# Optimization experiments

Measured on AMD Instinct MI355X. Metric: run time of the kernel, lower is better.

The kernel has to match this reference:

```python
import jax, jax.numpy as jnp
import numpy as np

EPSILON = 1e-8
MAX_WEIGHT = 0.15
N_ITER = 20
STEP_SIZE = 0.05
B, P = 32768, 45


def _simplex_projection(w):
    # clamp + renormalize, done twice (differentiable approximation)
    w = jnp.clip(w, 0.0, MAX_WEIGHT)
    w = w / (jnp.sum(w, axis=-1, keepdims=True) + EPSILON)
    w = jnp.clip(w, 0.0, MAX_WEIGHT)
    w = w / (jnp.sum(w, axis=-1, keepdims=True) + EPSILON)
    return w


def setup_inputs() -> dict:
    key = jax.random.key(0)
    k1, k2 = jax.random.split(key, 2)
    # SPD-ish covariance for a well-behaved iterative solve
    A = jax.random.normal(k1, (B, P, P), dtype=jnp.float32) * 0.1
    sigma = jnp.einsum('bij,bkj->bik', A, A) + 0.1 * jnp.eye(P, dtype=jnp.float32)
    beta = jax.nn.softmax(jax.random.normal(k2, (B, P), dtype=jnp.float32), axis=-1)
    w_prev = jnp.full((B, P), 1.0 / P, dtype=jnp.float32)
    return {
        'sigma': sigma,
        'beta': beta,
        'w_prev': w_prev,
        'log_lambda_sparse': jnp.asarray(-3.0, dtype=jnp.float32),
        'log_lambda_turnover': jnp.asarray(-2.0, dtype=jnp.float32),
    }


def reference(sigma, beta, w_prev, log_lambda_sparse, log_lambda_turnover):
    Bb, Pp = beta.shape
    lam_s = jnp.exp(log_lambda_sparse)
    lam_t = jnp.exp(log_lambda_turnover)
    w0 = jnp.full((Bb, Pp), 1.0 / Pp, dtype=sigma.dtype)

    def step(w, _):
        Sw = jnp.einsum('bij,bj->bi', sigma, w)  # [B,P]
        grad = 2.0 * Sw - beta + lam_s * jnp.sign(w) + 2.0 * lam_t * (w - w_prev)
        w = _simplex_projection(w - STEP_SIZE * grad)
        return w, None

    w, _ = jax.lax.scan(step, w0, None, length=N_ITER)
    return w
```

## Files before the change

kernel.cpp:

```cpp
#include <hip/hip_runtime.h>
#include <math.h>

#define P 45
#define N_ITER 20

typedef float v2f __attribute__((ext_vector_type(2)));
typedef float v4f __attribute__((ext_vector_type(4)));

template<int CTRL>
__device__ __forceinline__ float dpp_add(float x) {
    int xi = __builtin_bit_cast(int, x);
    int yi = __builtin_amdgcn_update_dpp(0, xi, CTRL, 0xF, 0xF, true);
    return x + __builtin_bit_cast(float, yi);
}

__device__ __forceinline__ float wave_sum_bcast(float x) {
    x = dpp_add<0x111>(x);
    x = dpp_add<0x112>(x);
    x = dpp_add<0x114>(x);
    x = dpp_add<0x118>(x);
    x = dpp_add<0x142>(x);
    x = dpp_add<0x143>(x);
    int si = __builtin_amdgcn_readlane(__builtin_bit_cast(int, x), 63);
    return __builtin_bit_cast(float, si);
}

__device__ __forceinline__ float clamp015(float x) {
    return __builtin_amdgcn_fmed3f(x, 0.0f, 0.15f);
}

__global__ __launch_bounds__(64) void drb_kernel(
    const float* __restrict__ sigma,
    const float* __restrict__ beta,
    const float* __restrict__ w_prev,
    const float* __restrict__ lls,
    const float* __restrict__ llt,
    float* __restrict__ out)
{
    const int b    = blockIdx.x;
    const int lane = threadIdx.x;
    const bool active = lane < P;

    const float lam_s  = expf(lls[0]);
    const float lam_t2 = 2.0f * expf(llt[0]);

    float base = 0.0f;
    if (active) {
        base = -beta[(size_t)b * P + lane]
               - lam_t2 * w_prev[(size_t)b * P + lane];
    }

    const int cidx = active ? lane : 0;
    const float* sp = sigma + (size_t)b * (P * P) + cidx;
    float rv[P + 1];
    #pragma unroll
    for (int j = 0; j < P; ++j) {
        float v = sp[(size_t)j * P];
        rv[j] = active ? v : 0.0f;
    }
    rv[P] = 0.0f;
    const bool ones = (lane == P);
    v2f row2[23];
    #pragma unroll
    for (int k = 0; k < 23; ++k) {
        float lo = ones ? 1.0f : rv[2 * k];
        float hi = (2 * k + 1 < P) ? (ones ? 1.0f : rv[2 * k + 1]) : 0.0f;
        v2f t; t.x = lo; t.y = hi;
        row2[k] = t;
    }
    #pragma unroll
    for (int k = 0; k < 23; ++k) asm volatile("" : "+v"(row2[k]));

    __shared__ __align__(16) float sh[128];

    float c = active ? (float)(1.0 / 45.0) : 0.0f;

    for (int it = 0; it < N_ITER; ++it) {
        float* shb = sh + ((it & 1) << 6);
        shb[lane] = c;
        __syncthreads();
        const v4f* shv = (const v4f*)shb;

        v2f acc0; acc0.x = 0.0f; acc0.y = 0.0f;
        v2f acc1 = acc0, acc2 = acc0;
        #pragma unroll
        for (int k = 0; k < 11; ++k) {
            v4f q = shv[k];
            v2f lo; lo.x = q.x; lo.y = q.y;
            v2f hi; hi.x = q.z; hi.y = q.w;
            acc0 = __builtin_elementwise_fma(row2[2 * k],     lo, acc0);
            acc1 = __builtin_elementwise_fma(row2[2 * k + 1], hi, acc1);
        }
        {
            v4f q = shv[11];
            v2f lo; lo.x = q.x; lo.y = q.y;
            acc2 = __builtin_elementwise_fma(row2[22], lo, acc2);
        }
        v2f am = acc0 + acc1;
        am = am + acc2;
        const float acc = am.x + am.y;

        const float s2 = __builtin_bit_cast(float,
            __builtin_amdgcn_readlane(__builtin_bit_cast(int, acc), P));
        const float r = __builtin_amdgcn_rcpf(s2 + 1e-8f);

        const float t = c * r;
        float g = fmaf(lam_t2, t, base);
        g += (c > 0.0f) ? lam_s : 0.0f;
        g = fmaf(r + r, acc, g);
        const float x = fmaf(-0.05f, g, t);

        const float a  = clamp015(x);
        const float s1 = wave_sum_bcast(a);
        const float r1 = __builtin_amdgcn_rcpf(s1 + 1e-8f);
        c = clamp015(a * r1);
    }

    const float sf = wave_sum_bcast(c);
    const float rf = __builtin_amdgcn_rcpf(sf + 1e-8f);
    if (active) out[(size_t)b * P + lane] = c * rf;
}

extern "C" void kernel_launch(void* const* d_in, const int* in_sizes, int n_in,
                              void* d_out, int out_size, void* d_ws, size_t ws_size,
                              hipStream_t stream) {
    const float* sigma  = (const float*)d_in[0];
    const float* beta   = (const float*)d_in[1];
    const float* w_prev = (const float*)d_in[2];
    const float* lls    = (const float*)d_in[3];
    const float* llt    = (const float*)d_in[4];
    float* out = (float*)d_out;

    const int B = in_sizes[1] / P;
    drb_kernel<<<B, 64, 0, stream>>>(sigma, beta, w_prev, lls, llt, out);
}
```

Baseline: 376.1 us.

## Process eight batch elements per workgroup in a persistent loop

Each 64-thread workgroup now handles eight batch elements in sequence instead of one, so the grid shrinks eightfold. This is meant to amortise workgroup launch and setup costs such as the lambda exps. The dot product is also split over four accumulators instead of three to shorten FMA dependency chains. The risk is that the sigma loads for each element are no longer overlapped by other resident workgroups unless occupancy is high, so memory latency may be exposed serially.

```diff
diff --git a/kernel.cpp b/kernel.cpp
--- a/kernel.cpp
+++ b/kernel.cpp
@@ -3,6 +3,7 @@
 
 #define P 45
 #define N_ITER 20
+#define EPW 8
 
 typedef float v2f __attribute__((ext_vector_type(2)));
 typedef float v4f __attribute__((ext_vector_type(4)));
@@ -35,90 +36,99 @@
     const float* __restrict__ w_prev,
     const float* __restrict__ lls,
     const float* __restrict__ llt,
-    float* __restrict__ out)
+    float* __restrict__ out,
+    int B)
 {
-    const int b    = blockIdx.x;
-    const int lane = threadIdx.x;
+    const int lane  = threadIdx.x;
     const bool active = lane < P;
+    const bool ones   = (lane == P);
+    const int  cidx   = active ? lane : 0;
 
     const float lam_s  = expf(lls[0]);
     const float lam_t2 = 2.0f * expf(llt[0]);
 
-    float base = 0.0f;
-    if (active) {
-        base = -beta[(size_t)b * P + lane]
-               - lam_t2 * w_prev[(size_t)b * P + lane];
-    }
-
-    const int cidx = active ? lane : 0;
-    const float* sp = sigma + (size_t)b * (P * P) + cidx;
-    float rv[P + 1];
-    #pragma unroll
-    for (int j = 0; j < P; ++j) {
-        float v = sp[(size_t)j * P];
-        rv[j] = active ? v : 0.0f;
-    }
-    rv[P] = 0.0f;
-    const bool ones = (lane == P);
-    v2f row2[23];
-    #pragma unroll
-    for (int k = 0; k < 23; ++k) {
-        float lo = ones ? 1.0f : rv[2 * k];
-        float hi = (2 * k + 1 < P) ? (ones ? 1.0f : rv[2 * k + 1]) : 0.0f;
-        v2f t; t.x = lo; t.y = hi;
-        row2[k] = t;
-    }
-    #pragma unroll
-    for (int k = 0; k < 23; ++k) asm volatile("" : "+v"(row2[k]));
-
     __shared__ __align__(16) float sh[128];
 
-    float c = active ? (float)(1.0 / 45.0) : 0.0f;
+    const int b0   = blockIdx.x * EPW;
+    const int bend = min(b0 + EPW, B);
 
-    for (int it = 0; it < N_ITER; ++it) {
-        float* shb = sh + ((it & 1) << 6);
-        shb[lane] = c;
-        __syncthreads();
-        const v4f* shv = (const v4f*)shb;
+    for (int b = b0; b < bend; ++b) {
+        float base = 0.0f;
+        if (active) {
+            base = -beta[(size_t)b * P + lane]
+                 - lam_t2 * w_prev[(size_t)b * P + lane];
+        }
 
-        v2f acc0; acc0.x = 0.0f; acc0.y = 0.0f;
-        v2f acc1 = acc0, acc2 = acc0;
+        const float* sp = sigma + (size_t)b * (P * P) + cidx;
+        float rv[P + 1];
         #pragma unroll
-        for (int k = 0; k < 11; ++k) {
-            v4f q = shv[k];
-            v2f lo; lo.x = q.x; lo.y = q.y;
-            v2f hi; hi.x = q.z; hi.y = q.w;
-            acc0 = __builtin_elementwise_fma(row2[2 * k],     lo, acc0);
-            acc1 = __builtin_elementwise_fma(row2[2 * k + 1], hi, acc1);
+        for (int j = 0; j < P; ++j) {
+            float v = sp[(size_t)j * P];
+            rv[j] = active ? v : 0.0f;
         }
-        {
-            v4f q = shv[11];
-            v2f lo; lo.x = q.x; lo.y = q.y;
-            acc2 = __builtin_elementwise_fma(row2[22], lo, acc2);
+        rv[P] = 0.0f;
+        v2f row2[23];
+        #pragma unroll
+        for (int k = 0; k < 23; ++k) {
+            float lo = ones ? 1.0f : rv[2 * k];
+            float hi = (2 * k + 1 < P) ? (ones ? 1.0f : rv[2 * k + 1]) : 0.0f;
+            v2f t; t.x = lo; t.y = hi;
+            row2[k] = t;
         }
-        v2f am = acc0 + acc1;
-        am = am + acc2;
-        const float acc = am.x + am.y;
+        #pragma unroll
+        for (int k = 0; k < 23; ++k) asm volatile("" : "+v"(row2[k]));
 
-        const float s2 = __builtin_bit_cast(float,
-            __builtin_amdgcn_readlane(__builtin_bit_cast(int, acc), P));
-        const float r = __builtin_amdgcn_rcpf(s2 + 1e-8f);
+        float c = active ? (float)(1.0 / 45.0) : 0.0f;
 
-        const float t = c * r;
-        float g = fmaf(lam_t2, t, base);
-        g += (c > 0.0f) ? lam_s : 0.0f;
-        g = fmaf(r + r, acc, g);
-        const float x = fmaf(-0.05f, g, t);
+        for (int it = 0; it < N_ITER; ++it) {
+            float* shb = sh + ((it & 1) << 6);
+            shb[lane] = c;
+            __syncthreads();
+            const v4f* shv = (const v4f*)shb;
 
-        const float a  = clamp015(x);
-        const float s1 = wave_sum_bcast(a);
-        const float r1 = __builtin_amdgcn_rcpf(s1 + 1e-8f);
-        c = clamp015(a * r1);
+            v2f accA; accA.x = 0.0f; accA.y = 0.0f;
+            v2f accB = accA, accC = accA, accD = accA;
+            #pragma unroll
+            for (int k = 0; k < 11; ++k) {
+                v4f q = shv[k];
+                v2f lo; lo.x = q.x; lo.y = q.y;
+                v2f hi; hi.x = q.z; hi.y = q.w;
+                if (k & 1) {
+                    accC = __builtin_elementwise_fma(row2[2 * k],     lo, accC);
+                    accD = __builtin_elementwise_fma(row2[2 * k + 1], hi, accD);
+                } else {
+                    accA = __builtin_elementwise_fma(row2[2 * k],     lo, accA);
+                    accB = __builtin_elementwise_fma(row2[2 * k + 1], hi, accB);
+                }
+            }
+            {
+                v4f q = shv[11];
+                v2f lo; lo.x = q.x; lo.y = q.y;
+                accC = __builtin_elementwise_fma(row2[22], lo, accC);
+            }
+            v2f am = (accA + accC) + (accB + accD);
+            const float acc = am.x + am.y;
+
+            const float s2 = __builtin_bit_cast(float,
+                __builtin_amdgcn_readlane(__builtin_bit_cast(int, acc), P));
+            const float r = __builtin_amdgcn_rcpf(s2 + 1e-8f);
+
+            const float t = c * r;
+            float g = fmaf(lam_t2, t, base);
+            g += (c > 0.0f) ? lam_s : 0.0f;
+            g = fmaf(r + r, acc, g);
+            const float x = fmaf(-0.05f, g, t);
+
+            const float a  = clamp015(x);
+            const float s1 = wave_sum_bcast(a);
+            const float r1 = __builtin_amdgcn_rcpf(s1 + 1e-8f);
+            c = clamp015(a * r1);
+        }
+
+        const float sf = wave_sum_bcast(c);
+        const float rf = __builtin_amdgcn_rcpf(sf + 1e-8f);
+        if (active) out[(size_t)b * P + lane] = c * rf;
     }
-
-    const float sf = wave_sum_bcast(c);
-    const float rf = __builtin_amdgcn_rcpf(sf + 1e-8f);
-    if (active) out[(size_t)b * P + lane] = c * rf;
 }
 
 extern "C" void kernel_launch(void* const* d_in, const int* in_sizes, int n_in,
@@ -132,5 +142,6 @@
     float* out = (float*)d_out;
 
     const int B = in_sizes[1] / P;
-    drb_kernel<<<B, 64, 0, stream>>>(sigma, beta, w_prev, lls, llt, out);
+    const int grid = (B + EPW - 1) / EPW;
+    drb_kernel<<<grid, 64, 0, stream>>>(sigma, beta, w_prev, lls, llt, out, B);
 }
```

Measured after the change: 390.1 us. 3.7% more time.
